# Performance work log

Measured on AMD Instinct MI355X. Metric: run time of the kernel, lower is better.

## Reference

```python
import jax, jax.numpy as jnp
import numpy as np


def setup_inputs() -> dict:
    key = jax.random.key(0)
    x = jax.random.normal(key, (32, 1024, 28, 28), dtype=jnp.float32)
    return {"x": x}


def reference(x):
    b, c, h, w = x.shape
    m = x.reshape(b, c, h * w)                       # [B, C, HW]
    scale = c ** -0.5
    # scores[b,i,j] = scale * <m[b,i,:], m[b,j,:]>  -> [B, C, C]
    scores = scale * jnp.einsum('bid,bjd->bij', m, m)
    attention = jax.nn.softmax(scores, axis=2)
    y = jnp.einsum('bij,bjd->bid', attention, m).reshape(b, c, h, w)
    return x + y
```

## Files before the change

kernel.cpp:

```cpp
#include <hip/hip_runtime.h>

typedef _Float16 f16;
typedef f16  half8 __attribute__((ext_vector_type(8)));
typedef float f32x4 __attribute__((ext_vector_type(4)));

#define B_   32
#define C_   1024
#define HW_  784
#define BQ   64

#define MA_BATCH  786432ull
#define TA_OFF    25165824ull
#define TA_BATCH  16384ull
#define MV_OFF    25690112ull
#define MV_BATCH  802816ull

__global__ __launch_bounds__(256)
void prep_kernel(const float* __restrict__ x, f16* __restrict__ ws) {
  __shared__ f16 lt[64][72];
  const int bi = blockIdx.x;
  const int ht = bi % 13;
  const int ct = (bi / 13) & 15;
  const int b  = bi / 208;
  const int h0 = ht * 64, c0 = ct * 64;
  const int t = threadIdx.x, r = t >> 2, q = t & 3;

  f16* mA = ws + (size_t)b * MA_BATCH;
  f16* tA = ws + TA_OFF + (size_t)b * TA_BATCH;
  f16* mV = ws + MV_OFF + (size_t)b * MV_BATCH;

  const int c  = c0 + r;
  const int pc = c >> 4, cl = c & 15;
  const int hq = h0 + q * 16;
  if (hq < HW_) {
    const float* src = x + (size_t)b * (C_ * HW_) + (size_t)c * HW_ + hq;
    float f[16];
#pragma unroll
    for (int j = 0; j < 4; ++j) ((float4*)f)[j] = ((const float4*)src)[j];
    f16 h[16];
#pragma unroll
    for (int j = 0; j < 16; ++j) h[j] = (f16)f[j];
    if (hq < 768) {
      const int kc = hq >> 5;
      const int l4 = (hq >> 3) & 3;
      f16* d0 = mA + ((size_t)pc * 24 + kc) * 512 + ((l4    ) * 16 + cl) * 8;
      f16* d1 = mA + ((size_t)pc * 24 + kc) * 512 + ((l4 + 1) * 16 + cl) * 8;
      *(half8*)d0 = *(half8*)h;
      *(half8*)d1 = *(half8*)(h + 8);
    } else {
      f16* d0 = tA + pc * 256 + cl * 8;
      f16* d1 = tA + pc * 256 + 128 + cl * 8;
      *(half8*)d0 = *(half8*)h;
      *(half8*)d1 = *(half8*)(h + 8);
    }
    *(half8*)&lt[r][q * 16]     = *(half8*)h;
    *(half8*)&lt[r][q * 16 + 8] = *(half8*)(h + 8);
  }
  __syncthreads();
  if (h0 + r < HW_) {
    f16 g[16];
#pragma unroll
    for (int j = 0; j < 16; ++j) g[j] = lt[q * 16 + j][r];
    const int d  = h0 + r;
    const int pd = d >> 4, dl = d & 15;
    const int kv = c0 + q * 16;
    const int kt = kv >> 5;
    const int l4 = (kv >> 3) & 3;
    f16* e0 = mV + ((size_t)pd * 32 + kt) * 512 + ((l4    ) * 16 + dl) * 8;
    f16* e1 = mV + ((size_t)pd * 32 + kt) * 512 + ((l4 + 1) * 16 + dl) * 8;
    *(half8*)e0 = *(half8*)g;
    *(half8*)e1 = *(half8*)(g + 8);
  }
}

__global__ __launch_bounds__(1024, 4)
void chanattn_main(const float* __restrict__ x, const f16* __restrict__ ws,
                   float* __restrict__ out) {
  __shared__ f16 Pl[BQ * C_];
  char* Pb = (char*)Pl;

  const int bi   = blockIdx.x;
  const int slot = bi >> 3;
  const int b    = ((slot >> 4) << 3) | (bi & 7);
  const int rb   = slot & 15;
  const int q0   = rb * BQ;

  const int tid  = threadIdx.x;
  const int w    = tid >> 6;
  const int lane = tid & 63;
  const int l15  = lane & 15;
  const int l4   = lane >> 4;

  const f16* mA = ws + (size_t)b * MA_BATCH;
  const f16* tA = ws + TA_OFF + (size_t)b * TA_BATCH;
  const f16* mV = ws + MV_OFF + (size_t)b * MV_BATCH;

  const int pa = q0 >> 4;

  {
    f32x4 acc[4][4] = {};
    for (int kc = 0; kc < 24; ++kc) {
      half8 afr[4], bfr[4];
#pragma unroll
      for (int rf = 0; rf < 4; ++rf)
        afr[rf] = *(const half8*)(mA + ((size_t)(pa + rf) * 24 + kc) * 512 + lane * 8);
#pragma unroll
      for (int cf = 0; cf < 4; ++cf)
        bfr[cf] = *(const half8*)(mA + ((size_t)(w * 4 + cf) * 24 + kc) * 512 + lane * 8);
#pragma unroll
      for (int rf = 0; rf < 4; ++rf)
#pragma unroll
        for (int cf = 0; cf < 4; ++cf)
          acc[rf][cf] = __builtin_amdgcn_mfma_f32_16x16x32_f16(afr[rf], bfr[cf], acc[rf][cf], 0, 0, 0);
    }
    {
      half8 afr[4], bfr[4];
#pragma unroll
      for (int rf = 0; rf < 4; ++rf) {
        half8 v = {};
        if (l4 < 2) v = *(const half8*)(tA + (pa + rf) * 256 + lane * 8);
        afr[rf] = v;
      }
#pragma unroll
      for (int cf = 0; cf < 4; ++cf) {
        half8 v = {};
        if (l4 < 2) v = *(const half8*)(tA + (w * 4 + cf) * 256 + lane * 8);
        bfr[cf] = v;
      }
#pragma unroll
      for (int rf = 0; rf < 4; ++rf)
#pragma unroll
        for (int cf = 0; cf < 4; ++cf)
          acc[rf][cf] = __builtin_amdgcn_mfma_f32_16x16x32_f16(afr[rf], bfr[cf], acc[rf][cf], 0, 0, 0);
    }
#pragma unroll
    for (int rf = 0; rf < 4; ++rf)
#pragma unroll
      for (int cf = 0; cf < 4; ++cf)
#pragma unroll
        for (int r = 0; r < 4; ++r) {
          const int row = rf * 16 + l4 * 4 + r;
          const int col = w * 64 + cf * 16 + l15;
          int byte = row * 2048 + col * 2;
          byte ^= (row & 7) << 4;
          *(f16*)(Pb + byte) = (f16)acc[rf][cf][r];
        }
  }
  __syncthreads();

  {
    const float ksc = 0.045084223f;
    for (int rr = 0; rr < 4; ++rr) {
      const int row = w * 4 + rr;
      const int sw  = (row & 7) << 4;
      char* rbase = Pb + row * 2048;
      const int p0 = (lane * 16) ^ sw;
      half8 v0 = *(half8*)(rbase + p0);
      half8 v1 = *(half8*)(rbase + 1024 + p0);
      float f[16];
#pragma unroll
      for (int e = 0; e < 8; ++e) { f[e] = (float)v0[e]; f[e+8] = (float)v1[e]; }
      float mx = f[0];
#pragma unroll
      for (int e = 1; e < 16; ++e) mx = fmaxf(mx, f[e]);
      for (int d = 1; d < 64; d <<= 1) mx = fmaxf(mx, __shfl_xor(mx, d));
      float sum = 0.f;
#pragma unroll
      for (int e = 0; e < 16; ++e) { f[e] = exp2f((f[e] - mx) * ksc); sum += f[e]; }
      for (int d = 1; d < 64; d <<= 1) sum += __shfl_xor(sum, d);
      const float inv = 1.f / sum;
#pragma unroll
      for (int e = 0; e < 8; ++e) { v0[e] = (f16)(f[e]*inv); v1[e] = (f16)(f[e+8]*inv); }
      *(half8*)(rbase + p0) = v0;
      *(half8*)(rbase + 1024 + p0) = v1;
    }
  }
  __syncthreads();

  {
    f32x4 a2[4][4] = {};
    for (int t = 0; t < 16; ++t) {
      half8 afr[4][2];
#pragma unroll
      for (int rf = 0; rf < 4; ++rf)
#pragma unroll
        for (int kf = 0; kf < 2; ++kf) {
          const int row = rf * 16 + l15;
          int byte = row * 2048 + t * 128 + kf * 64 + (l4 << 4);
          byte ^= (row & 7) << 4;
          afr[rf][kf] = *(half8*)(Pb + byte);
        }
#pragma unroll
      for (int si = 0; si < 4; ++si) {
        const int s = w + 16 * si;
        if (s < 49) {
#pragma unroll
          for (int kf = 0; kf < 2; ++kf) {
            const half8 bfr = *(const half8*)(mV + ((size_t)s * 32 + t * 2 + kf) * 512 + lane * 8);
#pragma unroll
            for (int rf = 0; rf < 4; ++rf)
              a2[si][rf] = __builtin_amdgcn_mfma_f32_16x16x32_f16(afr[rf][kf], bfr, a2[si][rf], 0, 0, 0);
          }
        }
      }
    }
#pragma unroll
    for (int si = 0; si < 4; ++si) {
      const int s = w + 16 * si;
      if (s < 49) {
        const int d = s * 16 + l15;
#pragma unroll
        for (int rf = 0; rf < 4; ++rf)
#pragma unroll
          for (int r = 0; r < 4; ++r) {
            const size_t idx = (size_t)(b * C_ + q0 + rf * 16 + l4 * 4 + r) * HW_ + d;
            out[idx] = x[idx] + a2[si][rf][r];
          }
      }
    }
  }
}

__device__ __forceinline__ half8 pack8(const float4& a, const float4& b) {
  half8 r;
  r[0]=(f16)a.x; r[1]=(f16)a.y; r[2]=(f16)a.z; r[3]=(f16)a.w;
  r[4]=(f16)b.x; r[5]=(f16)b.y; r[6]=(f16)b.z; r[7]=(f16)b.w;
  return r;
}

__global__ __launch_bounds__(512, 2)
void chanattn_fallback(const float* __restrict__ x, float* __restrict__ out) {
  __shared__ f16 Pl[BQ * C_];
  const int bi   = blockIdx.x;
  const int slot = bi >> 3;
  const int b    = ((slot >> 4) << 3) | (bi & 7);
  const int rb   = slot & 15;
  const int q0   = rb * BQ;
  const int tid  = threadIdx.x;
  const int w    = tid >> 6;
  const int lane = tid & 63;
  const int l15  = lane & 15;
  const int l4   = lane >> 4;
  const float* mb = x + (size_t)b * (C_ * HW_);
  char* Pb = (char*)Pl;
  {
    const int cw = w * 128;
    for (int tile = 0; tile < 2; ++tile) {
      const int c0 = cw + tile * 64;
      f32x4 acc[4][4] = {};
      for (int kc = 0; kc < 25; ++kc) {
        const int k0 = kc * 32 + l4 * 8;
        const bool ok = (k0 < HW_);
        half8 afr[4], bfr[4];
#pragma unroll
        for (int rf = 0; rf < 4; ++rf) {
          if (ok) { const float4* p = (const float4*)(mb + (q0 + rf*16 + l15) * HW_ + k0); afr[rf] = pack8(p[0], p[1]); }
          else {
#pragma unroll
            for (int e = 0; e < 8; ++e) afr[rf][e] = (f16)0.f; }
        }
#pragma unroll
        for (int cf = 0; cf < 4; ++cf) {
          if (ok) { const float4* p = (const float4*)(mb + (c0 + cf*16 + l15) * HW_ + k0); bfr[cf] = pack8(p[0], p[1]); }
          else {
#pragma unroll
            for (int e = 0; e < 8; ++e) bfr[cf][e] = (f16)0.f; }
        }
#pragma unroll
        for (int rf = 0; rf < 4; ++rf)
#pragma unroll
          for (int cf = 0; cf < 4; ++cf)
            acc[rf][cf] = __builtin_amdgcn_mfma_f32_16x16x32_f16(afr[rf], bfr[cf], acc[rf][cf], 0, 0, 0);
      }
#pragma unroll
      for (int rf = 0; rf < 4; ++rf)
#pragma unroll
        for (int cf = 0; cf < 4; ++cf)
#pragma unroll
          for (int r = 0; r < 4; ++r) {
            const int row = rf*16 + l4*4 + r;
            const int col = c0 + cf*16 + l15;
            int byte = row*2048 + col*2;
            byte ^= (row & 7) << 4;
            *(f16*)(Pb + byte) = (f16)acc[rf][cf][r];
          }
    }
  }
  __syncthreads();
  {
    const float ksc = 0.045084223f;
    for (int rr = 0; rr < 8; ++rr) {
      const int row = w*8 + rr;
      const int sw  = (row & 7) << 4;
      char* rbase = Pb + row*2048;
      const int p0 = (lane * 16) ^ sw;
      half8 v0 = *(half8*)(rbase + p0);
      half8 v1 = *(half8*)(rbase + 1024 + p0);
      float f[16];
#pragma unroll
      for (int e = 0; e < 8; ++e) { f[e] = (float)v0[e]; f[e+8] = (float)v1[e]; }
      float mx = f[0];
#pragma unroll
      for (int e = 1; e < 16; ++e) mx = fmaxf(mx, f[e]);
      for (int d = 1; d < 64; d <<= 1) mx = fmaxf(mx, __shfl_xor(mx, d));
      float sum = 0.f;
#pragma unroll
      for (int e = 0; e < 16; ++e) { f[e] = exp2f((f[e] - mx) * ksc); sum += f[e]; }
      for (int d = 1; d < 64; d <<= 1) sum += __shfl_xor(sum, d);
      const float inv = 1.f / sum;
#pragma unroll
      for (int e = 0; e < 8; ++e) { v0[e] = (f16)(f[e]*inv); v1[e] = (f16)(f[e+8]*inv); }
      *(half8*)(rbase + p0) = v0;
      *(half8*)(rbase + 1024 + p0) = v1;
    }
  }
  __syncthreads();
  {
    f32x4 acc[7][4] = {};
    for (int t = 0; t < 16; ++t) {
      half8 afr[4][2];
#pragma unroll
      for (int rf = 0; rf < 4; ++rf)
#pragma unroll
        for (int kf = 0; kf < 2; ++kf) {
          const int row = rf*16 + l15;
          int byte = row*2048 + t*128 + kf*64 + l4*16;
          byte ^= (row & 7) << 4;
          afr[rf][kf] = *(half8*)(Pb + byte);
        }
#pragma unroll
      for (int si = 0; si < 7; ++si) {
        const int s = w + 8*si;
        if (s < 49) {
          const int d = s*16 + l15;
#pragma unroll
          for (int kf = 0; kf < 2; ++kf) {
            const int kv = t*64 + kf*32 + l4*8;
            half8 bfr;
#pragma unroll
            for (int e = 0; e < 8; ++e) bfr[e] = (f16)mb[(kv + e) * HW_ + d];
#pragma unroll
            for (int rf = 0; rf < 4; ++rf)
              acc[si][rf] = __builtin_amdgcn_mfma_f32_16x16x32_f16(afr[rf][kf], bfr, acc[si][rf], 0, 0, 0);
          }
        }
      }
    }
#pragma unroll
    for (int si = 0; si < 7; ++si) {
      const int s = w + 8*si;
      if (s < 49) {
        const int d = s*16 + l15;
#pragma unroll
        for (int rf = 0; rf < 4; ++rf)
#pragma unroll
          for (int r = 0; r < 4; ++r) {
            const size_t idx = (size_t)(b*C_ + q0 + rf*16 + l4*4 + r) * HW_ + d;
            out[idx] = x[idx] + acc[si][rf][r];
          }
      }
    }
  }
}

extern "C" void kernel_launch(void* const* d_in, const int* in_sizes, int n_in,
                              void* d_out, int out_size, void* d_ws, size_t ws_size,
                              hipStream_t stream) {
  const float* x = (const float*)d_in[0];
  float* out = (float*)d_out;
  const size_t need = (MV_OFF + 32ull * MV_BATCH) * 2;
  if (ws_size >= need) {
    f16* ws = (f16*)d_ws;
    prep_kernel<<<dim3(32 * 16 * 13), dim3(256), 0, stream>>>(x, ws);
    chanattn_main<<<dim3(512), dim3(1024), 0, stream>>>(x, ws, out);
  } else {
    chanattn_fallback<<<dim3(512), dim3(512), 0, stream>>>(x, out);
  }
}
```

Before: 195.1 us.

## Split fused attention kernel into QK-softmax and PV kernels via global P buffer

```diff
diff --git a/kernel.cpp b/kernel.cpp
--- a/kernel.cpp
+++ b/kernel.cpp
@@ -14,6 +14,8 @@
 #define TA_BATCH  16384ull
 #define MV_OFF    25690112ull
 #define MV_BATCH  802816ull
+#define P_OFF     51380224ull
+#define P_TILE    65536ull
 
 __global__ __launch_bounds__(256)
 void prep_kernel(const float* __restrict__ x, f16* __restrict__ ws) {
@@ -74,8 +76,7 @@
 }
 
 __global__ __launch_bounds__(1024, 4)
-void chanattn_main(const float* __restrict__ x, const f16* __restrict__ ws,
-                   float* __restrict__ out) {
+void chanattn_qk(const f16* __restrict__ ws, f16* __restrict__ pws) {
   __shared__ f16 Pl[BQ * C_];
   char* Pb = (char*)Pl;
 
@@ -93,8 +94,6 @@
 
   const f16* mA = ws + (size_t)b * MA_BATCH;
   const f16* tA = ws + TA_OFF + (size_t)b * TA_BATCH;
-  const f16* mV = ws + MV_OFF + (size_t)b * MV_BATCH;
-
   const int pa = q0 >> 4;
 
   {
@@ -148,6 +147,162 @@
   }
   __syncthreads();
 
+  {
+    const float ksc = 0.045084223f;
+    f16* ptile = pws + (size_t)(b * 16 + rb) * P_TILE;
+    for (int rr = 0; rr < 4; ++rr) {
+      const int row = w * 4 + rr;
+      const int sw  = (row & 7) << 4;
+      char* rbase = Pb + row * 2048;
+      const int p0 = (lane * 16) ^ sw;
+      half8 v0 = *(half8*)(rbase + p0);
+      half8 v1 = *(half8*)(rbase + 1024 + p0);
+      float f[16];
+#pragma unroll
+      for (int e = 0; e < 8; ++e) { f[e] = (float)v0[e]; f[e+8] = (float)v1[e]; }
+      float mx = f[0];
+#pragma unroll
+      for (int e = 1; e < 16; ++e) mx = fmaxf(mx, f[e]);
+      for (int d = 1; d < 64; d <<= 1) mx = fmaxf(mx, __shfl_xor(mx, d));
+      float sum = 0.f;
+#pragma unroll
+      for (int e = 0; e < 16; ++e) { f[e] = exp2f((f[e] - mx) * ksc); sum += f[e]; }
+      for (int d = 1; d < 64; d <<= 1) sum += __shfl_xor(sum, d);
+      const float inv = 1.f / sum;
+#pragma unroll
+      for (int e = 0; e < 8; ++e) { v0[e] = (f16)(f[e]*inv); v1[e] = (f16)(f[e+8]*inv); }
+      f16* dst = ptile + (size_t)row * C_ + lane * 8;
+      *(half8*)dst         = v0;
+      *(half8*)(dst + 512) = v1;
+    }
+  }
+}
+
+__global__ __launch_bounds__(256, 4)
+void chanattn_pv(const float* __restrict__ x, const f16* __restrict__ ws,
+                 const f16* __restrict__ pws, float* __restrict__ out) {
+  const int bi = blockIdx.x;
+  const int b  = ((bi >> 9) << 3) | (bi & 7);
+  const int rb = (bi >> 5) & 15;
+  const int qd = (bi >> 3) & 3;
+  const int q0 = rb * BQ;
+
+  const int tid  = threadIdx.x;
+  const int wl   = tid >> 6;
+  const int lane = tid & 63;
+  const int l15  = lane & 15;
+  const int l4   = lane >> 4;
+
+  const f16* mV = ws + MV_OFF + (size_t)b * MV_BATCH;
+  const f16* pB = pws + (size_t)(b * 16 + rb) * P_TILE;
+
+  for (int si = 0; si < 4; ++si) {
+    const int s = qd + 4 * wl + 16 * si;
+    if (s >= 49) break;
+    const int d = s * 16 + l15;
+    const f16* vB = mV + (size_t)s * 32 * 512;
+    f32x4 a2[4] = {};
+    for (int t = 0; t < 16; ++t) {
+      half8 afr[4];
+#pragma unroll
+      for (int rf = 0; rf < 4; ++rf)
+        afr[rf] = *(const half8*)(pB + (size_t)(rf * 16 + l15) * C_ + t * 64 + l4 * 8);
+      half8 afr2[4];
+#pragma unroll
+      for (int rf = 0; rf < 4; ++rf)
+        afr2[rf] = *(const half8*)(pB + (size_t)(rf * 16 + l15) * C_ + t * 64 + 32 + l4 * 8);
+      const half8 b0 = *(const half8*)(vB + (size_t)(t * 2    ) * 512 + lane * 8);
+      const half8 b1 = *(const half8*)(vB + (size_t)(t * 2 + 1) * 512 + lane * 8);
+#pragma unroll
+      for (int rf = 0; rf < 4; ++rf)
+        a2[rf] = __builtin_amdgcn_mfma_f32_16x16x32_f16(afr[rf], b0, a2[rf], 0, 0, 0);
+#pragma unroll
+      for (int rf = 0; rf < 4; ++rf)
+        a2[rf] = __builtin_amdgcn_mfma_f32_16x16x32_f16(afr2[rf], b1, a2[rf], 0, 0, 0);
+    }
+#pragma unroll
+    for (int rf = 0; rf < 4; ++rf)
+#pragma unroll
+      for (int r = 0; r < 4; ++r) {
+        const size_t idx = (size_t)(b * C_ + q0 + rf * 16 + l4 * 4 + r) * HW_ + d;
+        out[idx] = x[idx] + a2[rf][r];
+      }
+  }
+}
+
+__global__ __launch_bounds__(1024, 4)
+void chanattn_mono(const float* __restrict__ x, const f16* __restrict__ ws,
+                   float* __restrict__ out) {
+  __shared__ f16 Pl[BQ * C_];
+  char* Pb = (char*)Pl;
+
+  const int bi   = blockIdx.x;
+  const int slot = bi >> 3;
+  const int b    = ((slot >> 4) << 3) | (bi & 7);
+  const int rb   = slot & 15;
+  const int q0   = rb * BQ;
+
+  const int tid  = threadIdx.x;
+  const int w    = tid >> 6;
+  const int lane = tid & 63;
+  const int l15  = lane & 15;
+  const int l4   = lane >> 4;
+
+  const f16* mA = ws + (size_t)b * MA_BATCH;
+  const f16* tA = ws + TA_OFF + (size_t)b * TA_BATCH;
+  const f16* mV = ws + MV_OFF + (size_t)b * MV_BATCH;
+  const int pa = q0 >> 4;
+
+  {
+    f32x4 acc[4][4] = {};
+    for (int kc = 0; kc < 24; ++kc) {
+      half8 afr[4], bfr[4];
+#pragma unroll
+      for (int rf = 0; rf < 4; ++rf)
+        afr[rf] = *(const half8*)(mA + ((size_t)(pa + rf) * 24 + kc) * 512 + lane * 8);
+#pragma unroll
+      for (int cf = 0; cf < 4; ++cf)
+        bfr[cf] = *(const half8*)(mA + ((size_t)(w * 4 + cf) * 24 + kc) * 512 + lane * 8);
+#pragma unroll
+      for (int rf = 0; rf < 4; ++rf)
+#pragma unroll
+        for (int cf = 0; cf < 4; ++cf)
+          acc[rf][cf] = __builtin_amdgcn_mfma_f32_16x16x32_f16(afr[rf], bfr[cf], acc[rf][cf], 0, 0, 0);
+    }
+    {
+      half8 afr[4], bfr[4];
+#pragma unroll
+      for (int rf = 0; rf < 4; ++rf) {
+        half8 v = {};
+        if (l4 < 2) v = *(const half8*)(tA + (pa + rf) * 256 + lane * 8);
+        afr[rf] = v;
+      }
+#pragma unroll
+      for (int cf = 0; cf < 4; ++cf) {
+        half8 v = {};
+        if (l4 < 2) v = *(const half8*)(tA + (w * 4 + cf) * 256 + lane * 8);
+        bfr[cf] = v;
+      }
+#pragma unroll
+      for (int rf = 0; rf < 4; ++rf)
+#pragma unroll
+        for (int cf = 0; cf < 4; ++cf)
+          acc[rf][cf] = __builtin_amdgcn_mfma_f32_16x16x32_f16(afr[rf], bfr[cf], acc[rf][cf], 0, 0, 0);
+    }
+#pragma unroll
+    for (int rf = 0; rf < 4; ++rf)
+#pragma unroll
+      for (int cf = 0; cf < 4; ++cf)
+#pragma unroll
+        for (int r = 0; r < 4; ++r) {
+          const int row = rf * 16 + l4 * 4 + r;
+          const int col = w * 64 + cf * 16 + l15;
+          int byte = row * 2048 + col * 2;
+          byte ^= (row & 7) << 4;
+          *(f16*)(Pb + byte) = (f16)acc[rf][cf][r];
+        }
+  }
+  __syncthreads();
   {
     const float ksc = 0.045084223f;
     for (int rr = 0; rr < 4; ++rr) {
@@ -176,7 +331,6 @@
     }
   }
   __syncthreads();
-
   {
     f32x4 a2[4][4] = {};
     for (int t = 0; t < 16; ++t) {
@@ -368,11 +522,18 @@
                               hipStream_t stream) {
   const float* x = (const float*)d_in[0];
   float* out = (float*)d_out;
-  const size_t need = (MV_OFF + 32ull * MV_BATCH) * 2;
-  if (ws_size >= need) {
+  const size_t need1 = P_OFF * 2;
+  const size_t need2 = (P_OFF + 512ull * P_TILE) * 2;
+  if (ws_size >= need2) {
+    f16* ws  = (f16*)d_ws;
+    f16* pws = ws + P_OFF;
+    prep_kernel<<<dim3(32 * 16 * 13), dim3(256), 0, stream>>>(x, ws);
+    chanattn_qk<<<dim3(512), dim3(1024), 0, stream>>>(ws, pws);
+    chanattn_pv<<<dim3(2048), dim3(256), 0, stream>>>(x, ws, pws, out);
+  } else if (ws_size >= need1) {
     f16* ws = (f16*)d_ws;
     prep_kernel<<<dim3(32 * 16 * 13), dim3(256), 0, stream>>>(x, ws);
-    chanattn_main<<<dim3(512), dim3(1024), 0, stream>>>(x, ws, out);
+    chanattn_mono<<<dim3(512), dim3(1024), 0, stream>>>(x, ws, out);
   } else {
     chanattn_fallback<<<dim3(512), dim3(512), 0, stream>>>(x, out);
   }
```

New measurement: 557.3 us. 186% more time.
